# Performance work log

Hardware: AMD Instinct MI355X
Metric: run time of the kernel (lower is better)

## Reference

```python
import jax, jax.numpy as jnp
import numpy as np

B, L, D = 2, 4096, 768
H, HD = 12, 64
EPS = 1e-6


def setup_inputs() -> dict:
    key = jax.random.key(0)
    ks = jax.random.split(key, 5)
    x = jax.random.normal(ks[0], (B, L, D), dtype=jnp.float32)
    # realistic rope tables
    inv_freq = 1.0 / (10000.0 ** (np.arange(0, HD, 2, dtype=np.float32) / HD))
    t = np.arange(L, dtype=np.float32)
    freqs = np.outer(t, inv_freq)  # (L, HD/2)
    emb = np.concatenate([freqs, freqs], axis=-1)  # (L, HD)
    rope_cos = jnp.asarray(np.cos(emb))
    rope_sin = jnp.asarray(np.sin(emb))
    Wqkv = jax.random.normal(ks[1], (3 * D, D), dtype=jnp.float32) * (1.0 / np.sqrt(D))
    Wout = jax.random.normal(ks[2], (D, D), dtype=jnp.float32) * (1.0 / np.sqrt(D))
    q_norm_w = jnp.ones((HD,), dtype=jnp.float32)
    k_norm_w = jnp.ones((HD,), dtype=jnp.float32)
    return {"x": x, "rope_cos": rope_cos, "rope_sin": rope_sin,
            "Wqkv": Wqkv, "Wout": Wout,
            "q_norm_w": q_norm_w, "k_norm_w": k_norm_w}


def _rms_norm(x, w):
    # x: (..., HD); computed in float32 like the torch module
    norm = jax.lax.rsqrt(jnp.mean(jnp.square(x.astype(jnp.float32)), axis=-1, keepdims=True) + EPS)
    return (x.astype(jnp.float32) * norm).astype(x.dtype) * w


def _rotate_half(x):
    x1, x2 = jnp.split(x, 2, axis=-1)
    return jnp.concatenate([-x2, x1], axis=-1)


def reference(x, rope_cos, rope_sin, Wqkv, Wout, q_norm_w, k_norm_w):
    b, l, d = x.shape
    # fused QKV projection (Linear with no bias): x @ Wqkv.T
    qkv = jnp.einsum('bld,ed->ble', x, Wqkv).reshape(b, l, 3, H, HD)
    q, k, v = qkv[:, :, 0], qkv[:, :, 1], qkv[:, :, 2]  # (B, L, H, HD)
    q = jnp.transpose(q, (0, 2, 1, 3))  # (B, H, L, HD)
    k = jnp.transpose(k, (0, 2, 1, 3))
    v = jnp.transpose(v, (0, 2, 1, 3))
    # per-head RMSNorm on q and k
    q = _rms_norm(q, q_norm_w)
    k = _rms_norm(k, k_norm_w)
    # RoPE: cos/sin (L, HD) broadcast over (B, H)
    cos = rope_cos[None, None, :, :]
    sin = rope_sin[None, None, :, :]
    q = q * cos + _rotate_half(q) * sin
    k = k * cos + _rotate_half(k) * sin
    # scaled dot product attention (no mask)
    scale = 1.0 / jnp.sqrt(jnp.asarray(HD, dtype=q.dtype))
    scores = jnp.einsum('bhqd,bhkd->bhqk', q, k) * scale  # (B, H, L, L)
    attn = jax.nn.softmax(scores, axis=-1)
    out = jnp.einsum('bhqk,bhkd->bhqd', attn, v)  # (B, H, L, HD)
    out = jnp.transpose(out, (0, 2, 1, 3)).reshape(b, l, d)
    return jnp.einsum('bld,ed->ble', out, Wout)
```

## Files before the change

### kernel.cpp

```cpp
#include <hip/hip_runtime.h>
#include <hip/hip_bf16.h>

typedef float f32x4 __attribute__((ext_vector_type(4)));
typedef short bf16x8 __attribute__((ext_vector_type(8)));
typedef unsigned short ushort8_t __attribute__((ext_vector_type(8)));

#define L_SEQ 4096
#define DMODEL 768
#define NHEAD 12
#define HDIM 64
#define QSCALE (0.125f * 1.44269504f)

__device__ __forceinline__ unsigned short f2bf(float f) {
    __hip_bfloat16 h = __float2bfloat16(f);
    return *reinterpret_cast<unsigned short*>(&h);
}

__device__ __forceinline__ unsigned pack2bf(float a, float b) {
    return (unsigned)f2bf(a) | ((unsigned)f2bf(b) << 16);
}

__device__ __forceinline__ void gload16(const void* g, void* l) {
    __builtin_amdgcn_global_load_lds(
        (const __attribute__((address_space(1))) unsigned int*)g,
        (__attribute__((address_space(3))) unsigned int*)l, 16, 0, 0);
}

__global__ __launch_bounds__(256) void cvt_f32_bf16(
    const float* __restrict__ in, unsigned short* __restrict__ out, int n)
{
    int i = (blockIdx.x * 256 + threadIdx.x) * 4;
    if (i + 3 < n) {
        float4 v = *reinterpret_cast<const float4*>(in + i);
        ushort4 o;
        o.x = f2bf(v.x); o.y = f2bf(v.y); o.z = f2bf(v.z); o.w = f2bf(v.w);
        *reinterpret_cast<ushort4*>(out + i) = o;
    }
}

#define BM 128
#define BN 128
#define BKK 64

__global__ __launch_bounds__(256) void gemm_qkv_fused(
    const unsigned short* __restrict__ A, const unsigned short* __restrict__ Bt,
    const float* __restrict__ cosb, const float* __restrict__ sinb,
    const float* __restrict__ qw, const float* __restrict__ kw,
    unsigned short* __restrict__ Qb, unsigned short* __restrict__ Kb,
    unsigned short* __restrict__ Vt)
{
    __shared__ union SM {
        struct { unsigned short As[BM][BKK]; unsigned short Bs[BN][BKK]; } st;
        unsigned short ep[4][64][72];
    } sm;

    const int K = DMODEL, M_ = 2 * L_SEQ;
    const int tid  = threadIdx.x;
    const int lane = tid & 63;
    const int wid  = tid >> 6;
    const int r = lane & 15, g = lane >> 4;
    const int wr = wid >> 1, wc = wid & 1;
    const int m0 = blockIdx.y * BM;
    const int n0 = blockIdx.x * BN;
    (void)M_;

    f32x4 acc[4][4];
    for (int i = 0; i < 4; ++i)
        for (int j = 0; j < 4; ++j)
            acc[i][j] = (f32x4){0.f, 0.f, 0.f, 0.f};

    for (int kt = 0; kt < K; kt += BKK) {
        __syncthreads();
        for (int p = 0; p < 4; ++p) {
            int idx = wid * 64 + p * 256 + lane;
            int row = idx >> 3;
            int ch  = (idx & 7) * 8;
            gload16(&A[(size_t)(m0 + row) * K + kt + ch],
                    (char*)sm.st.As + (size_t)(wid * 64 + p * 256) * 16);
            gload16(&Bt[(size_t)(n0 + row) * K + kt + ch],
                    (char*)sm.st.Bs + (size_t)(wid * 64 + p * 256) * 16);
        }
        __syncthreads();
        for (int k0 = 0; k0 < BKK; k0 += 32) {
            bf16x8 a[4], b[4];
            for (int i = 0; i < 4; ++i)
                a[i] = *reinterpret_cast<const bf16x8*>(&sm.st.As[wr * 64 + i * 16 + r][k0 + 8 * g]);
            for (int j = 0; j < 4; ++j)
                b[j] = *reinterpret_cast<const bf16x8*>(&sm.st.Bs[wc * 64 + j * 16 + r][k0 + 8 * g]);
            for (int i = 0; i < 4; ++i)
                for (int j = 0; j < 4; ++j)
                    acc[i][j] = __builtin_amdgcn_mfma_f32_16x16x32_bf16(a[i], b[j], acc[i][j], 0, 0, 0);
        }
    }

    __syncthreads();

    const int e0  = n0 + wc * 64;
    const int sec = e0 / DMODEL;
    const int h   = (e0 % DMODEL) / HDIM;
    const int row0 = m0 + wr * 64;
    const int b   = row0 >> 12;
    const int l0  = row0 & (L_SEQ - 1);
    unsigned short (*ep)[72] = sm.ep[wid];

    if (sec < 2) {
        const float* nw = (sec == 0) ? qw : kw;
        float wv[4];
        for (int j = 0; j < 4; ++j) wv[j] = nw[j * 16 + r];
        for (int i = 0; i < 4; ++i) {
            for (int t = 0; t < 4; ++t) {
                float ss = acc[i][0][t] * acc[i][0][t] + acc[i][1][t] * acc[i][1][t]
                         + acc[i][2][t] * acc[i][2][t] + acc[i][3][t] * acc[i][3][t];
                ss += __shfl_xor(ss, 1);
                ss += __shfl_xor(ss, 2);
                ss += __shfl_xor(ss, 4);
                ss += __shfl_xor(ss, 8);
                float inv = rsqrtf(ss * (1.f / 64.f) + 1e-6f);
                int lr = i * 16 + 4 * g + t;
                int l  = l0 + lr;
                float qn[4];
                for (int j = 0; j < 4; ++j) qn[j] = acc[i][j][t] * inv * wv[j];
                for (int j = 0; j < 4; ++j) {
                    int d = j * 16 + r;
                    float c = cosb[l * HDIM + d], s = sinb[l * HDIM + d];
                    float sgn = (j < 2) ? -1.f : 1.f;
                    float res = qn[j] * c + sgn * qn[j ^ 2] * s;
                    if (sec == 0) res *= QSCALE;
                    ep[lr][d] = f2bf(res);
                }
            }
        }
        unsigned short* dst = ((sec == 0) ? Qb : Kb)
            + ((size_t)(b * NHEAD + h) * L_SEQ + l0) * HDIM;
        for (int it = 0; it < 8; ++it) {
            int idx = it * 64 + lane;
            int lr = idx >> 3, ch = (idx & 7) * 8;
            ushort8_t v = *reinterpret_cast<const ushort8_t*>(&ep[lr][ch]);
            *reinterpret_cast<ushort8_t*>(&dst[(size_t)lr * HDIM + ch]) = v;
        }
    } else {
        for (int i = 0; i < 4; ++i)
            for (int t = 0; t < 4; ++t) {
                int lr = i * 16 + 4 * g + t;
                for (int j = 0; j < 4; ++j)
                    ep[j * 16 + r][lr] = f2bf(acc[i][j][t]);
            }
        unsigned short* dst = Vt + ((size_t)(b * NHEAD + h) * HDIM) * L_SEQ + l0;
        for (int it = 0; it < 8; ++it) {
            int idx = it * 64 + lane;
            int d = idx >> 3, ch = (idx & 7) * 8;
            ushort8_t v = *reinterpret_cast<const ushort8_t*>(&ep[d][ch]);
            *reinterpret_cast<ushort8_t*>(&dst[(size_t)d * L_SEQ + ch]) = v;
        }
    }
}

__global__ __launch_bounds__(256) void gemm_bf16_nt(
    const unsigned short* __restrict__ A, const unsigned short* __restrict__ Bt,
    float* __restrict__ C, int M, int N, int K)
{
    __shared__ unsigned short As[BM][BKK];
    __shared__ unsigned short Bs[BN][BKK];
    const int tid  = threadIdx.x;
    const int lane = tid & 63;
    const int wid  = tid >> 6;
    const int r = lane & 15, g = lane >> 4;
    const int wr = wid >> 1, wc = wid & 1;
    const int m0 = blockIdx.y * BM;
    const int n0 = blockIdx.x * BN;

    f32x4 acc[4][4];
    for (int i = 0; i < 4; ++i)
        for (int j = 0; j < 4; ++j)
            acc[i][j] = (f32x4){0.f, 0.f, 0.f, 0.f};

    for (int kt = 0; kt < K; kt += BKK) {
        __syncthreads();
        for (int p = 0; p < 4; ++p) {
            int idx = wid * 64 + p * 256 + lane;
            int row = idx >> 3;
            int ch  = (idx & 7) * 8;
            gload16(&A[(size_t)(m0 + row) * K + kt + ch],
                    (char*)As + (size_t)(wid * 64 + p * 256) * 16);
            gload16(&Bt[(size_t)(n0 + row) * K + kt + ch],
                    (char*)Bs + (size_t)(wid * 64 + p * 256) * 16);
        }
        __syncthreads();
        for (int k0 = 0; k0 < BKK; k0 += 32) {
            bf16x8 a[4], b[4];
            for (int i = 0; i < 4; ++i)
                a[i] = *reinterpret_cast<const bf16x8*>(&As[wr * 64 + i * 16 + r][k0 + 8 * g]);
            for (int j = 0; j < 4; ++j)
                b[j] = *reinterpret_cast<const bf16x8*>(&Bs[wc * 64 + j * 16 + r][k0 + 8 * g]);
            for (int i = 0; i < 4; ++i)
                for (int j = 0; j < 4; ++j)
                    acc[i][j] = __builtin_amdgcn_mfma_f32_16x16x32_bf16(a[i], b[j], acc[i][j], 0, 0, 0);
        }
    }
    for (int i = 0; i < 4; ++i)
        for (int j = 0; j < 4; ++j)
            for (int t = 0; t < 4; ++t) {
                int row = m0 + wr * 64 + i * 16 + 4 * g + t;
                int col = n0 + wc * 64 + j * 16 + r;
                C[(size_t)row * N + col] = acc[i][j][t];
            }
}

__global__ __launch_bounds__(256, 3) void flashattn(
    const unsigned short* __restrict__ Qb, const unsigned short* __restrict__ Kb,
    const unsigned short* __restrict__ Vt, unsigned short* __restrict__ aob)
{
    __shared__ unsigned short Ks[2][64 * 64];
    __shared__ unsigned short Vs[2][64 * 64];
    __shared__ unsigned short Ps[4][32 * 64];

    const int bh = blockIdx.y;
    const int b = bh / NHEAD, h = bh % NHEAD;
    const int tid = threadIdx.x;
    const int wid = tid >> 6, lane = tid & 63;
    const int r = lane & 15, g = lane >> 4;
    const int q0 = blockIdx.x * 128 + wid * 32;
    const int rsw = (r & 7) << 4;

    bf16x8 qf[2][2];
    for (int i = 0; i < 2; ++i) {
        const unsigned short* Qp = Qb + ((size_t)bh * L_SEQ + q0 + i * 16 + r) * HDIM + 8 * g;
        qf[i][0] = *reinterpret_cast<const bf16x8*>(Qp);
        qf[i][1] = *reinterpret_cast<const bf16x8*>(Qp + 32);
    }

    bf16x8 onesf;
    for (int e = 0; e < 8; ++e) onesf[e] = (r == 0) ? (short)0x3F80 : (short)0;

    const unsigned short* Kbase = Kb + (size_t)bh * L_SEQ * HDIM;
    const unsigned short* Vbase = Vt + (size_t)bh * HDIM * L_SEQ;
    char* PsB = (char*)Ps[wid];

    f32x4 o[2][4];
    for (int i = 0; i < 2; ++i)
        for (int j = 0; j < 4; ++j) o[i][j] = (f32x4){0.f, 0.f, 0.f, 0.f};
    f32x4 o_l[2];
    o_l[0] = (f32x4){0.f, 0.f, 0.f, 0.f};
    o_l[1] = (f32x4){0.f, 0.f, 0.f, 0.f};

    auto stage = [&](int buf, int kb) {
        for (int p = 0; p < 2; ++p) {
            int idx = wid * 64 + p * 256 + lane;
            int row = idx >> 3;
            int colb = ((idx & 7) * 16) ^ ((row & 7) << 4);
            gload16(Kbase + (size_t)(kb + row) * HDIM + (colb >> 1),
                    (char*)Ks[buf] + (size_t)(wid * 64 + p * 256) * 16);
            gload16(Vbase + (size_t)row * L_SEQ + kb + (colb >> 1),
                    (char*)Vs[buf] + (size_t)(wid * 64 + p * 256) * 16);
        }
    };

    stage(0, 0);
    __syncthreads();
    int cur = 0;

    for (int kb = 0; kb < L_SEQ; kb += 64) {
        if (kb + 64 < L_SEQ) stage(cur ^ 1, kb + 64);
        char* KsB = (char*)Ks[cur];
        char* VsB = (char*)Vs[cur];

        f32x4 s[2][4];
        for (int i = 0; i < 2; ++i)
            for (int kt = 0; kt < 4; ++kt) s[i][kt] = (f32x4){0.f, 0.f, 0.f, 0.f};
        __builtin_amdgcn_s_setprio(1);
        for (int kt = 0; kt < 4; ++kt) {
            bf16x8 kf0 = *reinterpret_cast<const bf16x8*>(KsB + (kt * 16 + r) * 128 + ((16 * g) ^ rsw));
            bf16x8 kf1 = *reinterpret_cast<const bf16x8*>(KsB + (kt * 16 + r) * 128 + ((64 + 16 * g) ^ rsw));
            for (int i = 0; i < 2; ++i) {
                s[i][kt] = __builtin_amdgcn_mfma_f32_16x16x32_bf16(kf0, qf[i][0], s[i][kt], 0, 0, 0);
                s[i][kt] = __builtin_amdgcn_mfma_f32_16x16x32_bf16(kf1, qf[i][1], s[i][kt], 0, 0, 0);
            }
        }
        __builtin_amdgcn_s_setprio(0);

        for (int i = 0; i < 2; ++i) {
            for (int kt = 0; kt < 4; ++kt) {
                float p0 = __builtin_amdgcn_exp2f(s[i][kt][0]);
                float p1 = __builtin_amdgcn_exp2f(s[i][kt][1]);
                float p2 = __builtin_amdgcn_exp2f(s[i][kt][2]);
                float p3 = __builtin_amdgcn_exp2f(s[i][kt][3]);
                uint2 w2;
                w2.x = pack2bf(p0, p1);
                w2.y = pack2bf(p2, p3);
                int dst = (i * 16 + r) * 128 + ((kt * 32 + 8 * g) ^ rsw);
                *reinterpret_cast<uint2*>(PsB + dst) = w2;
            }
        }

        bf16x8 pa[2][2];
        for (int i = 0; i < 2; ++i) {
            pa[i][0] = *reinterpret_cast<const bf16x8*>(PsB + (i * 16 + r) * 128 + ((16 * g) ^ rsw));
            pa[i][1] = *reinterpret_cast<const bf16x8*>(PsB + (i * 16 + r) * 128 + ((64 + 16 * g) ^ rsw));
        }
        __builtin_amdgcn_s_setprio(1);
        for (int i = 0; i < 2; ++i) {
            o_l[i] = __builtin_amdgcn_mfma_f32_16x16x32_bf16(pa[i][0], onesf, o_l[i], 0, 0, 0);
            o_l[i] = __builtin_amdgcn_mfma_f32_16x16x32_bf16(pa[i][1], onesf, o_l[i], 0, 0, 0);
        }
        for (int j = 0; j < 4; ++j) {
            bf16x8 vf0 = *reinterpret_cast<const bf16x8*>(VsB + (j * 16 + r) * 128 + ((16 * g) ^ rsw));
            bf16x8 vf1 = *reinterpret_cast<const bf16x8*>(VsB + (j * 16 + r) * 128 + ((64 + 16 * g) ^ rsw));
            for (int i = 0; i < 2; ++i) {
                o[i][j] = __builtin_amdgcn_mfma_f32_16x16x32_bf16(pa[i][0], vf0, o[i][j], 0, 0, 0);
                o[i][j] = __builtin_amdgcn_mfma_f32_16x16x32_bf16(pa[i][1], vf1, o[i][j], 0, 0, 0);
            }
        }
        __builtin_amdgcn_s_setprio(0);
        __syncthreads();
        cur ^= 1;
    }

    for (int i = 0; i < 2; ++i) {
        float i0 = 1.f / __shfl(o_l[i][0], 16 * g);
        float i1 = 1.f / __shfl(o_l[i][1], 16 * g);
        float i2 = 1.f / __shfl(o_l[i][2], 16 * g);
        float i3 = 1.f / __shfl(o_l[i][3], 16 * g);
        for (int j = 0; j < 4; ++j) {
            size_t base = ((size_t)(b * L_SEQ + q0 + i * 16 + 4 * g)) * DMODEL + h * HDIM + j * 16 + r;
            aob[base] = f2bf(o[i][j][0] * i0);
            aob[base + DMODEL] = f2bf(o[i][j][1] * i1);
            aob[base + 2 * DMODEL] = f2bf(o[i][j][2] * i2);
            aob[base + 3 * DMODEL] = f2bf(o[i][j][3] * i3);
        }
    }
}

extern "C" void kernel_launch(void* const* d_in, const int* in_sizes, int n_in,
                              void* d_out, int out_size, void* d_ws, size_t ws_size,
                              hipStream_t stream) {
    const float* x        = (const float*)d_in[0];
    const float* rope_cos = (const float*)d_in[1];
    const float* rope_sin = (const float*)d_in[2];
    const float* Wqkv     = (const float*)d_in[3];
    const float* Wout     = (const float*)d_in[4];
    const float* q_norm_w = (const float*)d_in[5];
    const float* k_norm_w = (const float*)d_in[6];
    float* out = (float*)d_out;

    const int BL = 2 * L_SEQ;
    const int nx    = BL * DMODEL;
    const int nwqkv = 3 * DMODEL * DMODEL;
    const int nwout = DMODEL * DMODEL;

    char* w = (char*)d_ws;
    unsigned short* xb    = (unsigned short*)w; w += (size_t)nx * 2;
    unsigned short* wqkvb = (unsigned short*)w; w += (size_t)nwqkv * 2;
    unsigned short* woutb = (unsigned short*)w; w += (size_t)nwout * 2;
    unsigned short* Qb    = (unsigned short*)w; w += (size_t)nx * 2;
    unsigned short* Kb    = (unsigned short*)w; w += (size_t)nx * 2;
    unsigned short* Vtb   = (unsigned short*)w; w += (size_t)nx * 2;
    unsigned short* aob   = (unsigned short*)w; w += (size_t)nx * 2;

    cvt_f32_bf16<<<nx / 1024, 256, 0, stream>>>(x, xb, nx);
    cvt_f32_bf16<<<nwqkv / 1024, 256, 0, stream>>>(Wqkv, wqkvb, nwqkv);
    cvt_f32_bf16<<<nwout / 1024, 256, 0, stream>>>(Wout, woutb, nwout);

    {
        dim3 grid(3 * DMODEL / BN, BL / BM);
        gemm_qkv_fused<<<grid, 256, 0, stream>>>(xb, wqkvb, rope_cos, rope_sin,
                                                 q_norm_w, k_norm_w, Qb, Kb, Vtb);
    }

    {
        dim3 grid(L_SEQ / 128, 24);
        flashattn<<<grid, 256, 0, stream>>>(Qb, Kb, Vtb, aob);
    }

    {
        dim3 grid(DMODEL / BN, BL / BM);
        gemm_bf16_nt<<<grid, 256, 0, stream>>>(aob, woutb, out, BL, DMODEL, DMODEL);
    }
}
```

Before: 222.5 us.

## Use 32x32 MFMA in attention with register P via permlane swap

Rewrites the attention inner loop to use 32x32x16 bf16 MFMA tiles, keeping the probability matrix in registers by rearranging it with v_permlane32_swap instead of round-tripping through shared memory. It also remaps the block index so consecutive blocks cycle through heads, which changes how K/V tiles are shared in cache. The three f32-to-bf16 conversion launches are merged into one. The aim is to remove LDS traffic and cut MFMA instruction count, at the cost of more live registers per thread.

New measurement: 230.9 us. +3.8%, slower.

```diff
diff --git a/kernel.cpp b/kernel.cpp
--- a/kernel.cpp
+++ b/kernel.cpp
@@ -2,6 +2,7 @@
 #include <hip/hip_bf16.h>
 
 typedef float f32x4 __attribute__((ext_vector_type(4)));
+typedef float f32x16 __attribute__((ext_vector_type(16)));
 typedef short bf16x8 __attribute__((ext_vector_type(8)));
 typedef unsigned short ushort8_t __attribute__((ext_vector_type(8)));
 
@@ -26,16 +27,21 @@
         (__attribute__((address_space(3))) unsigned int*)l, 16, 0, 0);
 }
 
-__global__ __launch_bounds__(256) void cvt_f32_bf16(
-    const float* __restrict__ in, unsigned short* __restrict__ out, int n)
+__global__ __launch_bounds__(256) void cvt3_f32_bf16(
+    const float* __restrict__ a, unsigned short* __restrict__ oa, int na,
+    const float* __restrict__ bsrc, unsigned short* __restrict__ ob, int nb,
+    const float* __restrict__ csrc, unsigned short* __restrict__ oc, int nc)
 {
     int i = (blockIdx.x * 256 + threadIdx.x) * 4;
-    if (i + 3 < n) {
-        float4 v = *reinterpret_cast<const float4*>(in + i);
-        ushort4 o;
-        o.x = f2bf(v.x); o.y = f2bf(v.y); o.z = f2bf(v.z); o.w = f2bf(v.w);
-        *reinterpret_cast<ushort4*>(out + i) = o;
-    }
+    const float* in; unsigned short* out;
+    if (i < na) { in = a; out = oa; }
+    else if (i < na + nb) { in = bsrc; out = ob; i -= na; }
+    else if (i < na + nb + nc) { in = csrc; out = oc; i -= na + nb; }
+    else return;
+    float4 v = *reinterpret_cast<const float4*>(in + i);
+    ushort4 o;
+    o.x = f2bf(v.x); o.y = f2bf(v.y); o.z = f2bf(v.z); o.w = f2bf(v.w);
+    *reinterpret_cast<ushort4*>(out + i) = o;
 }
 
 #define BM 128
@@ -54,7 +60,7 @@
         unsigned short ep[4][64][72];
     } sm;
 
-    const int K = DMODEL, M_ = 2 * L_SEQ;
+    const int K = DMODEL;
     const int tid  = threadIdx.x;
     const int lane = tid & 63;
     const int wid  = tid >> 6;
@@ -62,7 +68,6 @@
     const int wr = wid >> 1, wc = wid & 1;
     const int m0 = blockIdx.y * BM;
     const int n0 = blockIdx.x * BN;
-    (void)M_;
 
     f32x4 acc[4][4];
     for (int i = 0; i < 4; ++i)
@@ -212,36 +217,31 @@
 {
     __shared__ unsigned short Ks[2][64 * 64];
     __shared__ unsigned short Vs[2][64 * 64];
-    __shared__ unsigned short Ps[4][32 * 64];
-
-    const int bh = blockIdx.y;
+
+    const int lin = blockIdx.x;
+    const int bh = (lin & 7) + 8 * (lin >> 8);
+    const int qblk = (lin >> 3) & 31;
     const int b = bh / NHEAD, h = bh % NHEAD;
     const int tid = threadIdx.x;
     const int wid = tid >> 6, lane = tid & 63;
-    const int r = lane & 15, g = lane >> 4;
-    const int q0 = blockIdx.x * 128 + wid * 32;
-    const int rsw = (r & 7) << 4;
-
-    bf16x8 qf[2][2];
-    for (int i = 0; i < 2; ++i) {
-        const unsigned short* Qp = Qb + ((size_t)bh * L_SEQ + q0 + i * 16 + r) * HDIM + 8 * g;
-        qf[i][0] = *reinterpret_cast<const bf16x8*>(Qp);
-        qf[i][1] = *reinterpret_cast<const bf16x8*>(Qp + 32);
+    const int l31 = lane & 31, half = lane >> 5;
+    const int q0 = qblk * 128 + wid * 32;
+
+    bf16x8 qf[4];
+    {
+        const unsigned short* Qp = Qb + ((size_t)bh * L_SEQ + q0 + l31) * HDIM + 8 * half;
+        for (int dt = 0; dt < 4; ++dt)
+            qf[dt] = *reinterpret_cast<const bf16x8*>(Qp + dt * 16);
     }
 
     bf16x8 onesf;
-    for (int e = 0; e < 8; ++e) onesf[e] = (r == 0) ? (short)0x3F80 : (short)0;
+    for (int e = 0; e < 8; ++e) onesf[e] = (l31 == 0) ? (short)0x3F80 : (short)0;
 
     const unsigned short* Kbase = Kb + (size_t)bh * L_SEQ * HDIM;
     const unsigned short* Vbase = Vt + (size_t)bh * HDIM * L_SEQ;
-    char* PsB = (char*)Ps[wid];
-
-    f32x4 o[2][4];
-    for (int i = 0; i < 2; ++i)
-        for (int j = 0; j < 4; ++j) o[i][j] = (f32x4){0.f, 0.f, 0.f, 0.f};
-    f32x4 o_l[2];
-    o_l[0] = (f32x4){0.f, 0.f, 0.f, 0.f};
-    o_l[1] = (f32x4){0.f, 0.f, 0.f, 0.f};
+
+    f32x16 o0 = {0.f}, o1 = {0.f}, o_l = {0.f};
+    for (int e = 0; e < 16; ++e) { o0[e] = 0.f; o1[e] = 0.f; o_l[e] = 0.f; }
 
     auto stage = [&](int buf, int kb) {
         for (int p = 0; p < 2; ++p) {
@@ -261,53 +261,53 @@
 
     for (int kb = 0; kb < L_SEQ; kb += 64) {
         if (kb + 64 < L_SEQ) stage(cur ^ 1, kb + 64);
-        char* KsB = (char*)Ks[cur];
-        char* VsB = (char*)Vs[cur];
-
-        f32x4 s[2][4];
-        for (int i = 0; i < 2; ++i)
-            for (int kt = 0; kt < 4; ++kt) s[i][kt] = (f32x4){0.f, 0.f, 0.f, 0.f};
+        const char* KsB = (const char*)Ks[cur];
+        const char* VsB = (const char*)Vs[cur];
+
+        f32x16 s0 = o_l, s1 = o_l;
+        for (int e = 0; e < 16; ++e) { s0[e] = 0.f; s1[e] = 0.f; }
         __builtin_amdgcn_s_setprio(1);
-        for (int kt = 0; kt < 4; ++kt) {
-            bf16x8 kf0 = *reinterpret_cast<const bf16x8*>(KsB + (kt * 16 + r) * 128 + ((16 * g) ^ rsw));
-            bf16x8 kf1 = *reinterpret_cast<const bf16x8*>(KsB + (kt * 16 + r) * 128 + ((64 + 16 * g) ^ rsw));
-            for (int i = 0; i < 2; ++i) {
-                s[i][kt] = __builtin_amdgcn_mfma_f32_16x16x32_bf16(kf0, qf[i][0], s[i][kt], 0, 0, 0);
-                s[i][kt] = __builtin_amdgcn_mfma_f32_16x16x32_bf16(kf1, qf[i][1], s[i][kt], 0, 0, 0);
+        for (int kh = 0; kh < 2; ++kh) {
+            int krow = kh * 32 + l31;
+            const char* rowp = KsB + krow * 128;
+            int sw = (krow & 7) << 4;
+            f32x16& s = kh ? s1 : s0;
+            for (int dt = 0; dt < 4; ++dt) {
+                bf16x8 kf = *reinterpret_cast<const bf16x8*>(rowp + ((dt * 32 + half * 16) ^ sw));
+                s = __builtin_amdgcn_mfma_f32_32x32x16_bf16(kf, qf[dt], s, 0, 0, 0);
             }
         }
         __builtin_amdgcn_s_setprio(0);
 
-        for (int i = 0; i < 2; ++i) {
+        bf16x8 pa[4];
+        for (int kh = 0; kh < 2; ++kh) {
+            const f32x16& s = kh ? s1 : s0;
+            float p[16];
+            for (int e = 0; e < 16; ++e) p[e] = __builtin_amdgcn_exp2f(s[e]);
+            for (int kk = 0; kk < 2; ++kk) {
+                unsigned A = pack2bf(p[8 * kk + 0], p[8 * kk + 1]);
+                unsigned Bp = pack2bf(p[8 * kk + 2], p[8 * kk + 3]);
+                unsigned C = pack2bf(p[8 * kk + 4], p[8 * kk + 5]);
+                unsigned D = pack2bf(p[8 * kk + 6], p[8 * kk + 7]);
+                asm volatile("v_permlane32_swap_b32 %0, %1" : "+v"(A), "+v"(C));
+                asm volatile("v_permlane32_swap_b32 %0, %1" : "+v"(Bp), "+v"(D));
+                union { unsigned u[4]; bf16x8 v; } t;
+                t.u[0] = A; t.u[1] = Bp; t.u[2] = C; t.u[3] = D;
+                pa[2 * kh + kk] = t.v;
+            }
+        }
+
+        __builtin_amdgcn_s_setprio(1);
+        for (int kt = 0; kt < 4; ++kt)
+            o_l = __builtin_amdgcn_mfma_f32_32x32x16_bf16(pa[kt], onesf, o_l, 0, 0, 0);
+        for (int dh = 0; dh < 2; ++dh) {
+            int drow = dh * 32 + l31;
+            const char* rowp = VsB + drow * 128;
+            int sw = (drow & 7) << 4;
+            f32x16& o = dh ? o1 : o0;
             for (int kt = 0; kt < 4; ++kt) {
-                float p0 = __builtin_amdgcn_exp2f(s[i][kt][0]);
-                float p1 = __builtin_amdgcn_exp2f(s[i][kt][1]);
-                float p2 = __builtin_amdgcn_exp2f(s[i][kt][2]);
-                float p3 = __builtin_amdgcn_exp2f(s[i][kt][3]);
-                uint2 w2;
-                w2.x = pack2bf(p0, p1);
-                w2.y = pack2bf(p2, p3);
-                int dst = (i * 16 + r) * 128 + ((kt * 32 + 8 * g) ^ rsw);
-                *reinterpret_cast<uint2*>(PsB + dst) = w2;
-            }
-        }
-
-        bf16x8 pa[2][2];
-        for (int i = 0; i < 2; ++i) {
-            pa[i][0] = *reinterpret_cast<const bf16x8*>(PsB + (i * 16 + r) * 128 + ((16 * g) ^ rsw));
-            pa[i][1] = *reinterpret_cast<const bf16x8*>(PsB + (i * 16 + r) * 128 + ((64 + 16 * g) ^ rsw));
-        }
-        __builtin_amdgcn_s_setprio(1);
-        for (int i = 0; i < 2; ++i) {
-            o_l[i] = __builtin_amdgcn_mfma_f32_16x16x32_bf16(pa[i][0], onesf, o_l[i], 0, 0, 0);
-            o_l[i] = __builtin_amdgcn_mfma_f32_16x16x32_bf16(pa[i][1], onesf, o_l[i], 0, 0, 0);
-        }
-        for (int j = 0; j < 4; ++j) {
-            bf16x8 vf0 = *reinterpret_cast<const bf16x8*>(VsB + (j * 16 + r) * 128 + ((16 * g) ^ rsw));
-            bf16x8 vf1 = *reinterpret_cast<const bf16x8*>(VsB + (j * 16 + r) * 128 + ((64 + 16 * g) ^ rsw));
-            for (int i = 0; i < 2; ++i) {
-                o[i][j] = __builtin_amdgcn_mfma_f32_16x16x32_bf16(pa[i][0], vf0, o[i][j], 0, 0, 0);
-                o[i][j] = __builtin_amdgcn_mfma_f32_16x16x32_bf16(pa[i][1], vf1, o[i][j], 0, 0, 0);
+                bf16x8 vf = *reinterpret_cast<const bf16x8*>(rowp + ((kt * 32 + half * 16) ^ sw));
+                o = __builtin_amdgcn_mfma_f32_32x32x16_bf16(pa[kt], vf, o, 0, 0, 0);
             }
         }
         __builtin_amdgcn_s_setprio(0);
@@ -315,18 +315,14 @@
         cur ^= 1;
     }
 
-    for (int i = 0; i < 2; ++i) {
-        float i0 = 1.f / __shfl(o_l[i][0], 16 * g);
-        float i1 = 1.f / __shfl(o_l[i][1], 16 * g);
-        float i2 = 1.f / __shfl(o_l[i][2], 16 * g);
-        float i3 = 1.f / __shfl(o_l[i][3], 16 * g);
-        for (int j = 0; j < 4; ++j) {
-            size_t base = ((size_t)(b * L_SEQ + q0 + i * 16 + 4 * g)) * DMODEL + h * HDIM + j * 16 + r;
-            aob[base] = f2bf(o[i][j][0] * i0);
-            aob[base + DMODEL] = f2bf(o[i][j][1] * i1);
-            aob[base + 2 * DMODEL] = f2bf(o[i][j][2] * i2);
-            aob[base + 3 * DMODEL] = f2bf(o[i][j][3] * i3);
-        }
+    float linv[16];
+    for (int j = 0; j < 16; ++j)
+        linv[j] = 1.f / __shfl(o_l[j], lane & 32);
+    for (int j = 0; j < 16; ++j) {
+        int q = (j & 3) + 8 * (j >> 2) + 4 * half;
+        size_t base = ((size_t)(b * L_SEQ + q0 + q)) * DMODEL + h * HDIM + l31;
+        aob[base] = f2bf(o0[j] * linv[j]);
+        aob[base + 32] = f2bf(o1[j] * linv[j]);
     }
 }
 
@@ -356,9 +352,11 @@
     unsigned short* Vtb   = (unsigned short*)w; w += (size_t)nx * 2;
     unsigned short* aob   = (unsigned short*)w; w += (size_t)nx * 2;
 
-    cvt_f32_bf16<<<nx / 1024, 256, 0, stream>>>(x, xb, nx);
-    cvt_f32_bf16<<<nwqkv / 1024, 256, 0, stream>>>(Wqkv, wqkvb, nwqkv);
-    cvt_f32_bf16<<<nwout / 1024, 256, 0, stream>>>(Wout, woutb, nwout);
+    {
+        int total = (nx + nwqkv + nwout) / 4;
+        cvt3_f32_bf16<<<(total + 255) / 256, 256, 0, stream>>>(
+            x, xb, nx, Wqkv, wqkvb, nwqkv, Wout, woutb, nwout);
+    }
 
     {
         dim3 grid(3 * DMODEL / BN, BL / BM);
@@ -366,10 +364,7 @@
                                                  q_norm_w, k_norm_w, Qb, Kb, Vtb);
     }
 
-    {
-        dim3 grid(L_SEQ / 128, 24);
-        flashattn<<<grid, 256, 0, stream>>>(Qb, Kb, Vtb, aob);
-    }
+    flashattn<<<768, 256, 0, stream>>>(Qb, Kb, Vtb, aob);
 
     {
         dim3 grid(DMODEL / BN, BL / BM);
```
